# Kernel optimization log

Measured on AMD Instinct MI355X. Metric: run time of the kernel, lower is better.

Reference implementation:

```python
import math
import jax, jax.numpy as jnp
import numpy as np
from jax import lax

B, N, F = 16, 1024, 35  # graphs, nodes, one-hot label width
HID = 2000

def leaky(x):
    return jnp.where(x >= 0, x, 0.01 * x)

def spp(x, levels, mode):
    # x: [C,H,W]; faithful port of spatial_pyramid_pool.spp (per-level pool,
    # flatten, zero-pad to p*p). Pool params are static Python ints.
    C, H, W = x.shape
    outs = []
    for p in range(1, levels + 1):
        kh, kw = math.ceil(H / p), math.ceil(W / p)
        ph, pw = kh * p - H, kw * p - W
        if ph * 2 > kh:
            ph = kh // 2
        if pw * 2 > kw:
            pw = kw // 2
        pad = [(0, 0), (ph, ph), (pw, pw)]
        if mode == 'max':
            r = lax.reduce_window(x, -jnp.inf, lax.max, (1, kh, kw), (1, kh, kw), pad)
        else:  # avg, count_include_pad=True (torch default)
            r = lax.reduce_window(x, 0.0, lax.add, (1, kh, kw), (1, kh, kw), pad) / (kh * kw)
        flat = r.reshape(C, -1)
        flat = jnp.pad(flat, ((0, 0), (0, p * p - flat.shape[1])))
        outs.append(flat)
    return jnp.concatenate(outs, axis=1)  # [C, sum_p p^2]

def wlc(x, masks, K):
    # Vectorized weisfeiler_lehman_conv_switch.WLC.
    # x: [N,F]; masks: [4,N,N] one-hot of edge type s in {1..4}; K: [C,T,4,F].
    # Each convo step (snapshot semantics via cal_list.clone()):
    #   x_new[i] = x[i] + sum_j [s_ij==k+1] * x[j] * K[t,k]
    def one_channel(Kc):  # Kc: [T,4,F]
        def step(xc, Kt):
            return xc + jnp.einsum('kij,jf,kf->if', masks, xc, Kt), None
        xc, _ = lax.scan(step, x, Kc)
        return xc
    return jax.vmap(one_channel)(K)  # [C,N,F]

def conv2d(x, w, b):
    y = lax.conv_general_dilated(x, w, (1, 1), 'VALID',
                                 dimension_numbers=('NCHW', 'OIHW', 'NCHW'))
    return y + b[None, :, None, None]

def setup_inputs() -> dict:
    key = jax.random.key(0)
    ks = jax.random.split(key, 16)
    lin_in = 4 * sum((i + 1) ** 2 for i in range(10)) + 5 * sum((i + 1) ** 2 for i in range(3))  # 1610
    f32 = jnp.float32
    return {
        'labelsList': jax.random.normal(ks[0], (B, N, F), f32),
        'ligand_structure': jax.random.randint(ks[1], (B, N, N), 0, 5).astype(f32),
        'K1': jax.random.normal(ks[2], (2, 2, 4, F), f32) * 0.05,
        'K2': jax.random.normal(ks[3], (2, 2, 4, F), f32) * 0.05,
        'cw1': jax.random.normal(ks[4], (2, 1, 3, 3), f32) * 0.2,
        'cb1': jnp.zeros((2,), f32),
        'cw2': jax.random.normal(ks[5], (5, 2, 3, 3), f32) * 0.1,
        'cb2': jnp.zeros((5,), f32),
        'W1': jax.random.normal(ks[6], (HID, lin_in), f32) * 0.02,
        'b1': jnp.zeros((HID,), f32),
        'W2': jax.random.normal(ks[7], (HID, HID), f32) * 0.02,
        'b2': jnp.zeros((HID,), f32),
        'W3': jax.random.normal(ks[8], (HID, HID), f32) * 0.02,
        'b3': jnp.zeros((HID,), f32),
        'W4': jax.random.normal(ks[9], (HID, HID), f32) * 0.02,
        'b4': jnp.zeros((HID,), f32),
        'W5': jax.random.normal(ks[10], (2, HID), f32) * 0.02,
        'b5': jnp.zeros((2,), f32),
    }

def reference(labelsList, ligand_structure, K1, K2, cw1, cb1, cw2, cb2,
              W1, b1, W2, b2, W3, b3, W4, b4, W5, b5):
    def per_sample(x, s):  # x: [N,F], s: [N,N]
        masks = (s[None] == jnp.arange(1.0, 5.0, dtype=s.dtype)[:, None, None]).astype(x.dtype)
        c1 = leaky(wlc(x, masks, K1))                       # [2,N,F]
        c2 = jax.vmap(lambda xc: wlc(xc, masks, K2))(c1)    # [2,2,N,F], cat order matches torch
        c2 = c2.reshape(4, N, F)
        feat = spp(leaky(c2), 10, 'max').reshape(-1)        # [1540]
        z = s[None, None]                                   # [1,1,N,N]
        z = leaky(conv2d(z, cw1, cb1))
        z = leaky(conv2d(z, cw2, cb2))                      # [1,5,N-4,N-4]
        stru = spp(z[0], 3, 'avg').reshape(-1)              # [70]
        return jnp.concatenate([feat, stru])                # [1610]

    h = jax.vmap(per_sample)(labelsList, ligand_structure)  # [B,1610]
    # fc_model (dropout = identity in eval)
    h = leaky(h @ W1.T + b1)
    h = leaky(h @ W2.T + b2)
    h = leaky(h @ W3.T + b3)
    h = leaky(h @ W4.T + b4)
    return h @ W5.T + b5                                    # [B,2]
```

## Files before the change

kernel.cpp:

```cpp
#include <hip/hip_runtime.h>
#include <stdint.h>

#define NN 1024
#define FF 35
#define LIN_IN 1610
#define NB 16

typedef short short8 __attribute__((ext_vector_type(8)));
typedef float f32x4 __attribute__((ext_vector_type(4)));
typedef float f32x2 __attribute__((ext_vector_type(2)));

__device__ __forceinline__ float leakyf(float x) { return fmaxf(x, 0.01f * x); }
__device__ __forceinline__ uint16_t to_bf16(float v) {
    return (uint16_t)((__float_as_uint(v) + 0x8000u) >> 16);
}
__device__ __forceinline__ f32x2 sp2(float s) { return (f32x2){s, s}; }
__device__ __forceinline__ f32x2 leaky2(f32x2 v) {
    f32x2 r;
    r.x = fmaxf(v.x, 0.01f * v.x);
    r.y = fmaxf(v.y, 0.01f * v.y);
    return r;
}
__device__ __forceinline__ uint32_t mapf(float x) {
    uint32_t u = __float_as_uint(x);
    return (u & 0x80000000u) ? ~u : (u | 0x80000000u);
}
__device__ __forceinline__ float unmapf(uint32_t u) {
    return (u & 0x80000000u) ? __uint_as_float(u & 0x7FFFFFFFu) : __uint_as_float(~u);
}

__global__ __launch_bounds__(256)
void codes_kernel(const float* __restrict__ s, uint8_t* __restrict__ codes, int n4) {
    int i = blockIdx.x * 256 + threadIdx.x;
    for (; i < n4; i += gridDim.x * 256) {
        float4 v = ((const float4*)s)[i];
        uchar4 c;
        c.x = (uint8_t)v.x; c.y = (uint8_t)v.y; c.z = (uint8_t)v.z; c.w = (uint8_t)v.w;
        ((uchar4*)codes)[i] = c;
    }
}

__global__ __launch_bounds__(256)
void labels_to_xt(const float* __restrict__ labels, uint16_t* __restrict__ XT0,
                  float* __restrict__ XR0)
{
    __shared__ float buf[256 * FF];
    const int s = blockIdx.x;
    const int i0 = blockIdx.y * 256;
    const float* src = labels + ((size_t)s * NN + i0) * FF;
    for (int t = threadIdx.x; t < 256 * FF; t += 256) buf[t] = src[t];
    __syncthreads();
    for (int f = 0; f < 48; ++f) {
        const int ii = threadIdx.x;
        float v = (f < FF) ? buf[ii * FF + f] : 0.f;
        size_t o = ((size_t)s * 48 + f) * 1024 + i0 + ii;
        XR0[o] = v;
        XT0[o] = to_bf16(v);
    }
}

__device__ __forceinline__ short8 expand_onehot(uint2 cd, uint32_t dupK) {
    union { uint32_t u[4]; short8 v; } r;
#pragma unroll
    for (int h = 0; h < 2; ++h) {
        uint32_t d = h ? cd.y : cd.x;
        uint32_t y = d ^ dupK;
        uint32_t m = (~(((y & 0x7F7F7F7Fu) + 0x7F7F7F7Fu) | y)) & 0x80808080u;
        uint32_t m2 = m >> 7;
        r.u[h * 2 + 0] = ((m2 & 0xFFu) | ((m2 & 0xFF00u) << 8)) * 0x3F80u;
        r.u[h * 2 + 1] = (((m2 >> 16) & 0xFFu) | ((m2 >> 8) & 0xFF0000u)) * 0x3F80u;
    }
    return r.v;
}

__device__ __forceinline__
void wlc_body(int mt, int nt, int s,
              const uint16_t* __restrict__ XT_in, const float* __restrict__ XR_in,
              uint16_t* __restrict__ XT_out, float* __restrict__ XR_out,
              const uint8_t* __restrict__ codes, const float* __restrict__ Kg,
              int t, int shift, int nch_in, int nch_out, int do_leaky)
{
    const int tid   = threadIdx.x;
    const int wid   = tid >> 6;
    const int lane  = tid & 63;
    const int chout = nt;
    const int inch  = chout >> shift;
    const int kch   = chout & 1;
    const int i0    = mt * 64 + wid * 16;

    const uint8_t* cbase = codes + ((size_t)s << 20)
        + (size_t)(i0 + (lane & 15)) * 1024 + ((lane >> 4) << 3);
    const uint16_t* bbase = XT_in + (((size_t)s * nch_in + inch) * 48 + (lane & 15)) * 1024
        + ((lane >> 4) << 3);

    f32x4 acc[4][3];
#pragma unroll
    for (int k = 0; k < 4; ++k)
#pragma unroll
        for (int nf = 0; nf < 3; ++nf) acc[k][nf] = (f32x4){0.f, 0.f, 0.f, 0.f};

#pragma unroll 2
    for (int jt = 0; jt < 16; ++jt) {
        const int j0 = jt * 64;
        const uint2 cd0 = *(const uint2*)(cbase + j0);
        const uint2 cd1 = *(const uint2*)(cbase + j0 + 32);

        short8 bfr[3][2];
#pragma unroll
        for (int nf = 0; nf < 3; ++nf)
#pragma unroll
            for (int kk = 0; kk < 2; ++kk)
                bfr[nf][kk] = *(const short8*)(bbase + (size_t)nf * 16 * 1024 + j0 + kk * 32);

#pragma unroll
        for (int k = 0; k < 4; ++k) {
            const uint32_t dupK = 0x01010101u * (k + 1);
#pragma unroll
            for (int kk = 0; kk < 2; ++kk) {
                short8 af = expand_onehot(kk ? cd1 : cd0, dupK);
#pragma unroll
                for (int nf = 0; nf < 3; ++nf)
                    acc[k][nf] = __builtin_amdgcn_mfma_f32_16x16x32_bf16(
                        af, bfr[nf][kk], acc[k][nf], 0, 0, 0);
            }
        }
    }

    float sc[4][3];
#pragma unroll
    for (int nf = 0; nf < 3; ++nf) {
        int fnl = nf * 16 + (lane & 15);
#pragma unroll
        for (int k = 0; k < 4; ++k)
            sc[k][nf] = (fnl < FF) ? Kg[((kch * 2 + t) * 4 + k) * FF + fnl] : 0.f;
    }

#pragma unroll
    for (int nf = 0; nf < 3; ++nf) {
        int fnl = nf * 16 + (lane & 15);
        int irow = i0 + ((lane >> 4) << 2);
        f32x4 rr = sc[0][nf] * acc[0][nf];
        rr += sc[1][nf] * acc[1][nf];
        rr += sc[2][nf] * acc[2][nf];
        rr += sc[3][nf] * acc[3][nf];
        size_t rb = (((size_t)s * nch_in + inch) * 48 + fnl) * 1024 + irow;
        float4 rd = *(const float4*)&XR_in[rb];
        float y0 = rr.x + rd.x, y1 = rr.y + rd.y, y2 = rr.z + rd.z, y3 = rr.w + rd.w;
        if (do_leaky) { y0 = leakyf(y0); y1 = leakyf(y1); y2 = leakyf(y2); y3 = leakyf(y3); }
        size_t ob = (((size_t)s * nch_out + chout) * 48 + fnl) * 1024 + irow;
        *(float4*)&XR_out[ob] = make_float4(y0, y1, y2, y3);
        ushort4 bv;
        bv.x = to_bf16(y0); bv.y = to_bf16(y1); bv.z = to_bf16(y2); bv.w = to_bf16(y3);
        *(ushort4*)&XT_out[ob] = bv;
    }
}

__global__ __launch_bounds__(256, 2)
void wlc_gemm(const uint16_t* __restrict__ XT_in, const float* __restrict__ XR_in,
              uint16_t* __restrict__ XT_out, float* __restrict__ XR_out,
              const uint8_t* __restrict__ codes, const float* __restrict__ Kg,
              int t, int shift, int nch_in, int nch_out, int do_leaky)
{
    wlc_body(blockIdx.x, blockIdx.y, blockIdx.z, XT_in, XR_in, XT_out, XR_out,
             codes, Kg, t, shift, nch_in, nch_out, do_leaky);
}

__device__ __forceinline__
void conv_body(int ss, int simg,
               const float* __restrict__ sM,
               const float* __restrict__ cw1, const float* __restrict__ cb1,
               const float* __restrict__ cw2, const float* __restrict__ cb2,
               float* __restrict__ h0)
{
    __shared__ float bins[30];
    const int tid  = threadIdx.x;
    const int lane = tid & 63;
    const int r0   = ss * 17;
    const int rb2  = ss / 30;
    const int rb3  = ss / 20;

    if (tid < 30) bins[tid] = 0.f;
    __syncthreads();

    const int colbase = (tid < 255) ? tid * 4 : 254 * 4;
    const float* sp = sM + (size_t)simg * (NN * NN) + colbase;

    f32x2 w1p[9], w2p[45], b1p;
#pragma unroll
    for (int i = 0; i < 9; ++i) { w1p[i].x = cw1[i]; w1p[i].y = cw1[9 + i]; }
#pragma unroll
    for (int o = 0; o < 5; ++o)
#pragma unroll
        for (int i = 0; i < 9; ++i) {
            w2p[o * 9 + i].x = cw2[(o * 2 + 0) * 9 + i];
            w2p[o * 9 + i].y = cw2[(o * 2 + 1) * 9 + i];
        }
    b1p.x = cb1[0]; b1p.y = cb1[1];
    float b2r[5];
#pragma unroll
    for (int i = 0; i < 5; ++i) b2r[i] = cb2[i];

    float sw[3][8];
    f32x2 z1w[3][6];
    float acc[5][4];
#pragma unroll
    for (int o = 0; o < 5; ++o)
#pragma unroll
        for (int j = 0; j < 4; ++j) acc[o][j] = 0.f;

#define LOADROW(slot, rabs) do { \
    float4 v0 = *(const float4*)(sp + (size_t)(rabs) * NN); \
    float4 v1 = *(const float4*)(sp + (size_t)(rabs) * NN + 4); \
    sw[slot][0]=v0.x; sw[slot][1]=v0.y; sw[slot][2]=v0.z; sw[slot][3]=v0.w; \
    sw[slot][4]=v1.x; sw[slot][5]=v1.y; sw[slot][6]=v1.z; sw[slot][7]=v1.w; } while(0)

#define Z1ROW(P) do { \
    _Pragma("unroll") for (int jj = 0; jj < 6; ++jj) { \
        f32x2 a = b1p; \
        _Pragma("unroll") for (int dc = 0; dc < 3; ++dc) { \
            a += sp2(sw[((P)+2)%3][jj+dc]) * w1p[0+dc]; \
            a += sp2(sw[(P)%3    ][jj+dc]) * w1p[3+dc]; \
            a += sp2(sw[((P)+1)%3][jj+dc]) * w1p[6+dc]; } \
        z1w[((P)+2)%3][jj] = leaky2(a); } } while(0)

#define Z2ROW(P) do { \
    _Pragma("unroll") for (int o = 0; o < 5; ++o) { \
      _Pragma("unroll") for (int j = 0; j < 4; ++j) { \
        f32x2 a = (f32x2){b2r[o], 0.f}; \
        _Pragma("unroll") for (int dc = 0; dc < 3; ++dc) { \
            a += z1w[(P)%3    ][j+dc] * w2p[o*9+0+dc]; \
            a += z1w[((P)+1)%3][j+dc] * w2p[o*9+3+dc]; \
            a += z1w[((P)+2)%3][j+dc] * w2p[o*9+6+dc]; } \
        float sres = a.x + a.y; \
        acc[o][j] += fmaxf(sres, 0.01f * sres); } } } while(0)

    LOADROW(0, r0 + 0);
    LOADROW(1, r0 + 1);
    LOADROW(2, r0 + 2);
    Z1ROW(1);
    LOADROW(0, r0 + 3);
    Z1ROW(2);

#pragma unroll 1
    for (int rr = 0; rr < 15; rr += 3) {
        LOADROW(1, r0 + rr + 4); Z1ROW(0); Z2ROW(0);
        LOADROW(2, r0 + rr + 5); Z1ROW(1); Z2ROW(1);
        LOADROW(0, r0 + rr + 6); Z1ROW(2); Z2ROW(2);
    }
    LOADROW(1, r0 + 19); Z1ROW(0); Z2ROW(0);
    LOADROW(2, r0 + 20); Z1ROW(1); Z2ROW(1);

#undef LOADROW
#undef Z1ROW
#undef Z2ROW

    if (tid == 255) {
#pragma unroll
        for (int o = 0; o < 5; ++o)
#pragma unroll
            for (int j = 0; j < 4; ++j) acc[o][j] = 0.f;
    }

    int cb2c[4], cb3c[4];
#pragma unroll
    for (int j = 0; j < 4; ++j) {
        int col = colbase + j;
        int a2 = col / 510; if (a2 > 1) a2 = 1;
        int a3 = col / 340; if (a3 > 2) a3 = 2;
        cb2c[j] = a2; cb3c[j] = a3;
    }

#pragma unroll
    for (int o = 0; o < 5; ++o) {
        float t1 = acc[o][0] + acc[o][1] + acc[o][2] + acc[o][3];
        float pa = 0.f, pb = 0.f, q0 = 0.f, q1 = 0.f, q2 = 0.f;
#pragma unroll
        for (int j = 0; j < 4; ++j) {
            float v = acc[o][j];
            if (cb2c[j] == 0) pa += v; else pb += v;
            if (cb3c[j] == 0) q0 += v; else if (cb3c[j] == 1) q1 += v; else q2 += v;
        }
#pragma unroll
        for (int d = 32; d >= 1; d >>= 1) {
            t1 += __shfl_xor(t1, d, 64);
            pa += __shfl_xor(pa, d, 64);
            pb += __shfl_xor(pb, d, 64);
            q0 += __shfl_xor(q0, d, 64);
            q1 += __shfl_xor(q1, d, 64);
            q2 += __shfl_xor(q2, d, 64);
        }
        if (lane == 0) {
            atomicAdd(&bins[o * 6 + 0], t1);
            atomicAdd(&bins[o * 6 + 1], pa);
            atomicAdd(&bins[o * 6 + 2], pb);
            atomicAdd(&bins[o * 6 + 3], q0);
            atomicAdd(&bins[o * 6 + 4], q1);
            atomicAdd(&bins[o * 6 + 5], q2);
        }
    }
    __syncthreads();
    if (tid < 30) {
        int o = tid / 6, b = tid % 6;
        int off; float scale;
        if (b == 0)      { off = 0;                         scale = 1.f / (1020.f * 1020.f); }
        else if (b <= 2) { off = 1 + rb2 * 2 + (b - 1);     scale = 1.f / (510.f * 510.f); }
        else             { off = 5 + rb3 * 3 + (b - 3);     scale = 1.f / (340.f * 340.f); }
        atomicAdd(h0 + (size_t)simg * LIN_IN + 1540 + o * 14 + off, bins[tid] * scale);
    }
}

__global__ __launch_bounds__(256, 2)
void fused_wlc_conv(int convBlocks, int imgBase,
                    const float* __restrict__ sM,
                    const float* __restrict__ cw1, const float* __restrict__ cb1,
                    const float* __restrict__ cw2, const float* __restrict__ cb2,
                    float* __restrict__ h0,
                    const uint16_t* __restrict__ XT_in, const float* __restrict__ XR_in,
                    uint16_t* __restrict__ XT_out, float* __restrict__ XR_out,
                    const uint8_t* __restrict__ codes, const float* __restrict__ Kg,
                    int t, int shift, int nch_in, int nch_out, int do_leaky)
{
    const int bid = blockIdx.x;
    if (bid < convBlocks) {
        conv_body(bid % 60, imgBase + bid / 60, sM, cw1, cb1, cw2, cb2, h0);
    } else {
        const int b = bid - convBlocks;
        wlc_body(b & 15, (b >> 4) & 3, b >> 6, XT_in, XR_in, XT_out, XR_out,
                 codes, Kg, t, shift, nch_in, nch_out, do_leaky);
    }
}

__global__ __launch_bounds__(256)
void spp_scatter_kernel(const float* __restrict__ xr4, uint32_t* __restrict__ scratch)
{
    constexpr int KH[10] = {1024, 512, 342, 256, 205, 171, 147, 128, 114, 103};
    constexpr int PH[10] = {0, 0, 2, 0, 1, 2, 5, 0, 2, 6};
    constexpr int KW[10] = {35, 18, 12, 9, 7, 6, 5, 5, 4, 4};
    constexpr int PW[10] = {0, 1, 1, 1, 0, 1, 0, 2, 1, 2};
    constexpr int OW[10] = {1, 2, 3, 4, 5, 6, 7, 7, 9, 9};
    constexpr int BASE[10] = {0, 1, 5, 14, 30, 55, 91, 140, 204, 285};

    __shared__ uint32_t cells[385];
    const int b  = blockIdx.x;
    const int rq = b & 3;
    const int c  = (b >> 2) & 3;
    const int s  = b >> 4;
    const int r  = rq * 256 + threadIdx.x;

    for (int i = threadIdx.x; i < 385; i += 256) cells[i] = 0u;
    __syncthreads();

    const float* bp = xr4 + ((size_t)s * 4 + c) * (48 * 1024) + r;

    int addr[10];
#pragma unroll
    for (int pi = 0; pi < 10; ++pi)
        addr[pi] = BASE[pi] + ((r + PH[pi]) / KH[pi]) * OW[pi];

    float acc[10];
#pragma unroll
    for (int pi = 0; pi < 10; ++pi) acc[pi] = -3.402823466e38f;

#pragma unroll
    for (int f = 0; f < FF; ++f) {
        const float v = bp[(size_t)f * 1024];
#pragma unroll
        for (int pi = 0; pi < 10; ++pi) {
            const int cbin = (f + PW[pi]) / KW[pi];
            const int cbn  = (f + 1 < FF) ? ((f + 1 + PW[pi]) / KW[pi]) : -1;
            if (cbin < OW[pi]) {
                acc[pi] = fmaxf(acc[pi], v);
                if (cbn != cbin) {
                    atomicMax(&cells[addr[pi] + cbin], mapf(acc[pi]));
                    acc[pi] = -3.402823466e38f;
                }
            }
        }
    }

    __syncthreads();
    for (int i = threadIdx.x; i < 385; i += 256) {
        uint32_t u = cells[i];
        if (u) atomicMax(&scratch[((size_t)s * 4 + c) * 385 + i], u);
    }
}

__global__ __launch_bounds__(256)
void spp_unmap_kernel(const uint32_t* __restrict__ scratch, float* __restrict__ h0)
{
    constexpr int OHW[10] = {1, 4, 9, 16, 25, 36, 49, 56, 81, 90};
    const int idx = blockIdx.x * 256 + threadIdx.x;
    if (idx >= NB * 4 * 385) return;
    const int s = idx / (4 * 385);
    int rem = idx - s * (4 * 385);
    const int c = rem / 385;
    const int cell = rem - c * 385;

    int p1 = 1, base = 0;
    while (p1 < 10 && cell >= base + p1 * p1) { base += p1 * p1; ++p1; }
    const int ci = cell - base;
    if (ci >= OHW[p1 - 1]) return;

    h0[(size_t)s * LIN_IN + c * 385 + cell] = unmapf(scratch[idx]);
}

template<int VEC>
__global__ __launch_bounds__(256)
void fc_kernel(const float* __restrict__ in, const float* __restrict__ W,
               const float* __restrict__ bias, float* __restrict__ out,
               int K, int Nout, int do_leaky)
{
    const int o = (blockIdx.x * 256 + threadIdx.x) >> 6;
    const int lane = threadIdx.x & 63;
    if (o >= Nout) return;
    const float* wrow = W + (size_t)o * K;
    float acc[16];
#pragma unroll
    for (int b = 0; b < 16; ++b) acc[b] = 0.f;

    const int step = 64 * VEC;
    const int kmain = (K / step) * step;
#pragma unroll 2
    for (int k0 = 0; k0 < kmain; k0 += step) {
        const int kk = k0 + lane * VEC;
        if (VEC == 4) {
            float4 w = *(const float4*)(wrow + kk);
#pragma unroll
            for (int b = 0; b < 16; ++b) {
                float4 h = *(const float4*)(in + (size_t)b * K + kk);
                acc[b] += w.x * h.x + w.y * h.y + w.z * h.z + w.w * h.w;
            }
        } else {
            float2 w = *(const float2*)(wrow + kk);
#pragma unroll
            for (int b = 0; b < 16; ++b) {
                float2 h = *(const float2*)(in + (size_t)b * K + kk);
                acc[b] += w.x * h.x + w.y * h.y;
            }
        }
    }
    {
        const int kk = kmain + lane * VEC;
        if (kk < K) {
            if (VEC == 4) {
                float4 w = *(const float4*)(wrow + kk);
#pragma unroll
                for (int b = 0; b < 16; ++b) {
                    float4 h = *(const float4*)(in + (size_t)b * K + kk);
                    acc[b] += w.x * h.x + w.y * h.y + w.z * h.z + w.w * h.w;
                }
            } else {
                float2 w = *(const float2*)(wrow + kk);
#pragma unroll
                for (int b = 0; b < 16; ++b) {
                    float2 h = *(const float2*)(in + (size_t)b * K + kk);
                    acc[b] += w.x * h.x + w.y * h.y;
                }
            }
        }
    }

    float res = 0.f;
#pragma unroll
    for (int b = 0; b < 16; ++b) {
        float v = acc[b];
#pragma unroll
        for (int od = 32; od >= 1; od >>= 1) v += __shfl_xor(v, od, 64);
        if (lane == b) res = v;
    }
    if (lane < 16) {
        const float y = res + bias[o];
        out[(size_t)lane * Nout + o] = do_leaky ? leakyf(y) : y;
    }
}

extern "C" void kernel_launch(void* const* d_in, const int* in_sizes, int n_in,
                              void* d_out, int out_size, void* d_ws, size_t ws_size,
                              hipStream_t stream)
{
    const float* labels = (const float*)d_in[0];
    const float* sM     = (const float*)d_in[1];
    const float* K1     = (const float*)d_in[2];
    const float* K2     = (const float*)d_in[3];
    const float* cw1    = (const float*)d_in[4];
    const float* cb1    = (const float*)d_in[5];
    const float* cw2    = (const float*)d_in[6];
    const float* cb2    = (const float*)d_in[7];
    const float* W1     = (const float*)d_in[8];
    const float* b1     = (const float*)d_in[9];
    const float* W2     = (const float*)d_in[10];
    const float* b2     = (const float*)d_in[11];
    const float* W3     = (const float*)d_in[12];
    const float* b3     = (const float*)d_in[13];
    const float* W4     = (const float*)d_in[14];
    const float* b4     = (const float*)d_in[15];
    const float* W5     = (const float*)d_in[16];
    const float* b5     = (const float*)d_in[17];

    char* ws = (char*)d_ws;
    uint8_t* codes = (uint8_t*)ws;  ws += (size_t)16 << 20;
    char* ping = ws;                ws += 18874368;
    char* pong = ws;                ws += 18874368;
    float* h0  = (float*)ws;        ws += 103168;
    float* hA  = (float*)ws;        ws += 128000;
    float* hB  = (float*)ws;        ws += 128000;
    uint32_t* sppbuf = (uint32_t*)ws; ws += (size_t)NB * 4 * 385 * 4;

    uint16_t* XTp = (uint16_t*)ping; float* XRp = (float*)(ping + 6291456);
    uint16_t* XTq = (uint16_t*)pong; float* XRq = (float*)(pong + 6291456);

    hipMemsetAsync(h0, 0, (size_t)NB * LIN_IN * 4, stream);
    hipMemsetAsync(sppbuf, 0, (size_t)NB * 4 * 385 * 4, stream);

    codes_kernel<<<2048, 256, 0, stream>>>(sM, codes, 16 * 1024 * 1024 / 4);
    labels_to_xt<<<dim3(16, 4), 256, 0, stream>>>(labels, XTq, XRq);

    wlc_gemm<<<dim3(16, 2, 16), 256, 0, stream>>>(XTq, XRq, XTp, XRp, codes, K1, 0, 1, 1, 2, 0);
    wlc_gemm<<<dim3(16, 2, 16), 256, 0, stream>>>(XTp, XRp, XTq, XRq, codes, K1, 1, 0, 2, 2, 1);

    fused_wlc_conv<<<480 + 1024, 256, 0, stream>>>(
        480, 0, sM, cw1, cb1, cw2, cb2, h0,
        XTq, XRq, XTp, XRp, codes, K2, 0, 1, 2, 4, 0);
    fused_wlc_conv<<<480 + 1024, 256, 0, stream>>>(
        480, 8, sM, cw1, cb1, cw2, cb2, h0,
        XTp, XRp, XTq, XRq, codes, K2, 1, 0, 4, 4, 1);

    spp_scatter_kernel<<<256, 256, 0, stream>>>(XRq, sppbuf);
    spp_unmap_kernel<<<(NB * 4 * 385 + 255) / 256, 256, 0, stream>>>(sppbuf, h0);

    fc_kernel<2><<<500, 256, 0, stream>>>(h0, W1, b1, hA, LIN_IN, 2000, 1);
    fc_kernel<4><<<500, 256, 0, stream>>>(hA, W2, b2, hB, 2000, 2000, 1);
    fc_kernel<4><<<500, 256, 0, stream>>>(hB, W3, b3, hA, 2000, 2000, 1);
    fc_kernel<4><<<500, 256, 0, stream>>>(hA, W4, b4, hB, 2000, 2000, 1);
    fc_kernel<4><<<1,   256, 0, stream>>>(hB, W5, b5, (float*)d_out, 2000, 2, 0);
}
```

Before: 334.6 us.

## Stage WLC operands in LDS with prefetch, merge prep kernels, fuse SPP passes

The WLC GEMM body now stages each 64-wide slice of the bf16 feature tile and the edge-code tile in shared memory, using an XOR swizzle and register prefetch of the next slice. This replaces per-wave global loads, so the four waves share one copy. The codes and label-transpose kernels are merged into a single launch. The two-pass SPP (atomic scatter, then unmap) becomes one 1024-thread block per sample/channel that writes h0 directly, removing a memset and a launch. In exchange, the GEMM loop gains two barriers per iteration and uses more LDS, and the SPP kernel runs only 64 blocks.

```diff
diff --git a/kernel.cpp b/kernel.cpp
--- a/kernel.cpp
+++ b/kernel.cpp
@@ -30,32 +30,34 @@
 }
 
 __global__ __launch_bounds__(256)
-void codes_kernel(const float* __restrict__ s, uint8_t* __restrict__ codes, int n4) {
-    int i = blockIdx.x * 256 + threadIdx.x;
-    for (; i < n4; i += gridDim.x * 256) {
-        float4 v = ((const float4*)s)[i];
-        uchar4 c;
-        c.x = (uint8_t)v.x; c.y = (uint8_t)v.y; c.z = (uint8_t)v.z; c.w = (uint8_t)v.w;
-        ((uchar4*)codes)[i] = c;
-    }
-}
-
-__global__ __launch_bounds__(256)
-void labels_to_xt(const float* __restrict__ labels, uint16_t* __restrict__ XT0,
-                  float* __restrict__ XR0)
-{
-    __shared__ float buf[256 * FF];
-    const int s = blockIdx.x;
-    const int i0 = blockIdx.y * 256;
-    const float* src = labels + ((size_t)s * NN + i0) * FF;
-    for (int t = threadIdx.x; t < 256 * FF; t += 256) buf[t] = src[t];
-    __syncthreads();
-    for (int f = 0; f < 48; ++f) {
-        const int ii = threadIdx.x;
-        float v = (f < FF) ? buf[ii * FF + f] : 0.f;
-        size_t o = ((size_t)s * 48 + f) * 1024 + i0 + ii;
-        XR0[o] = v;
-        XT0[o] = to_bf16(v);
+void prep_kernel(const float* __restrict__ s, uint8_t* __restrict__ codes, int n4,
+                 const float* __restrict__ labels, uint16_t* __restrict__ XT0,
+                 float* __restrict__ XR0)
+{
+    const int bid = blockIdx.x;
+    if (bid < 2048) {
+        int i = bid * 256 + threadIdx.x;
+        for (; i < n4; i += 2048 * 256) {
+            float4 v = ((const float4*)s)[i];
+            uchar4 c;
+            c.x = (uint8_t)v.x; c.y = (uint8_t)v.y; c.z = (uint8_t)v.z; c.w = (uint8_t)v.w;
+            ((uchar4*)codes)[i] = c;
+        }
+    } else {
+        __shared__ float buf[256 * FF];
+        const int lb = bid - 2048;
+        const int si = lb >> 2;
+        const int i0 = (lb & 3) * 256;
+        const float* src = labels + ((size_t)si * NN + i0) * FF;
+        for (int t = threadIdx.x; t < 256 * FF; t += 256) buf[t] = src[t];
+        __syncthreads();
+        for (int f = 0; f < 48; ++f) {
+            const int ii = threadIdx.x;
+            float v = (f < FF) ? buf[ii * FF + f] : 0.f;
+            size_t o = ((size_t)si * 48 + f) * 1024 + i0 + ii;
+            XR0[o] = v;
+            XT0[o] = to_bf16(v);
+        }
     }
 }
 
@@ -80,18 +82,32 @@
               const uint8_t* __restrict__ codes, const float* __restrict__ Kg,
               int t, int shift, int nch_in, int nch_out, int do_leaky)
 {
+    __shared__ __align__(16) uint16_t xs[48 * 64];
+    __shared__ __align__(16) uint8_t  cds[64 * 80];
+
     const int tid   = threadIdx.x;
     const int wid   = tid >> 6;
     const int lane  = tid & 63;
     const int chout = nt;
     const int inch  = chout >> shift;
     const int kch   = chout & 1;
-    const int i0    = mt * 64 + wid * 16;
-
-    const uint8_t* cbase = codes + ((size_t)s << 20)
-        + (size_t)(i0 + (lane & 15)) * 1024 + ((lane >> 4) << 3);
-    const uint16_t* bbase = XT_in + (((size_t)s * nch_in + inch) * 48 + (lane & 15)) * 1024
-        + ((lane >> 4) << 3);
+    const int i0    = mt * 64;
+    const int irow0 = i0 + wid * 16;
+
+    const int u0 = tid, u1 = tid + 256;
+    const bool v1 = (u1 < 384);
+    const int r0s = u0 >> 3, c80 = u0 & 7;
+    const int r1s = u1 >> 3, c81 = u1 & 7;
+    const uint16_t* src0 = XT_in + (((size_t)s * nch_in + inch) * 48 + r0s) * 1024 + c80 * 8;
+    const uint16_t* src1 = XT_in + (((size_t)s * nch_in + inch) * 48 + (v1 ? r1s : 0)) * 1024 + c81 * 8;
+    uint16_t* dst0 = &xs[r0s * 64 + ((c80 ^ (r0s & 7)) * 8)];
+    uint16_t* dst1 = &xs[(v1 ? r1s : 0) * 64 + ((c81 ^ (r1s & 7)) * 8)];
+
+    const int crow = tid >> 2, ccol = (tid & 3) * 16;
+    const uint8_t* csrc = codes + ((size_t)s << 20) + (size_t)(i0 + crow) * 1024 + ccol;
+    uint8_t* cdst = &cds[crow * 80 + ccol];
+
+    const int cd_off = (wid * 16 + (lane & 15)) * 80 + ((lane >> 4) << 3);
 
     f32x4 acc[4][3];
 #pragma unroll
@@ -99,18 +115,36 @@
 #pragma unroll
         for (int nf = 0; nf < 3; ++nf) acc[k][nf] = (f32x4){0.f, 0.f, 0.f, 0.f};
 
-#pragma unroll 2
+    uint4 preB0 = *(const uint4*)src0;
+    uint4 preB1 = v1 ? *(const uint4*)src1 : (uint4){0, 0, 0, 0};
+    uint4 preC  = *(const uint4*)csrc;
+
     for (int jt = 0; jt < 16; ++jt) {
-        const int j0 = jt * 64;
-        const uint2 cd0 = *(const uint2*)(cbase + j0);
-        const uint2 cd1 = *(const uint2*)(cbase + j0 + 32);
+        __syncthreads();
+        *(uint4*)dst0 = preB0;
+        if (v1) *(uint4*)dst1 = preB1;
+        *(uint4*)cdst = preC;
+        __syncthreads();
+
+        if (jt < 15) {
+            const int j1 = (jt + 1) * 64;
+            preB0 = *(const uint4*)(src0 + j1);
+            if (v1) preB1 = *(const uint4*)(src1 + j1);
+            preC  = *(const uint4*)(csrc + j1);
+        }
+
+        const uint2 cd0 = *(const uint2*)&cds[cd_off];
+        const uint2 cd1 = *(const uint2*)&cds[cd_off + 32];
 
         short8 bfr[3][2];
 #pragma unroll
         for (int nf = 0; nf < 3; ++nf)
 #pragma unroll
-            for (int kk = 0; kk < 2; ++kk)
-                bfr[nf][kk] = *(const short8*)(bbase + (size_t)nf * 16 * 1024 + j0 + kk * 32);
+            for (int kk = 0; kk < 2; ++kk) {
+                int n = nf * 16 + (lane & 15);
+                int c8 = kk * 4 + (lane >> 4);
+                bfr[nf][kk] = *(const short8*)&xs[n * 64 + ((c8 ^ (n & 7)) * 8)];
+            }
 
 #pragma unroll
         for (int k = 0; k < 4; ++k) {
@@ -138,7 +172,7 @@
 #pragma unroll
     for (int nf = 0; nf < 3; ++nf) {
         int fnl = nf * 16 + (lane & 15);
-        int irow = i0 + ((lane >> 4) << 2);
+        int irow = irow0 + ((lane >> 4) << 2);
         f32x4 rr = sc[0][nf] * acc[0][nf];
         rr += sc[1][nf] * acc[1][nf];
         rr += sc[2][nf] * acc[2][nf];
@@ -324,30 +358,29 @@
     if (bid < convBlocks) {
         conv_body(bid % 60, imgBase + bid / 60, sM, cw1, cb1, cw2, cb2, h0);
     } else {
-        const int b = bid - convBlocks;
-        wlc_body(b & 15, (b >> 4) & 3, b >> 6, XT_in, XR_in, XT_out, XR_out,
+        const int w = bid - convBlocks;
+        wlc_body(w & 15, (w >> 4) & 3, w >> 6, XT_in, XR_in, XT_out, XR_out,
                  codes, Kg, t, shift, nch_in, nch_out, do_leaky);
     }
 }
 
-__global__ __launch_bounds__(256)
-void spp_scatter_kernel(const float* __restrict__ xr4, uint32_t* __restrict__ scratch)
+__global__ __launch_bounds__(1024)
+void spp_kernel(const float* __restrict__ xr4, float* __restrict__ h0)
 {
     constexpr int KH[10] = {1024, 512, 342, 256, 205, 171, 147, 128, 114, 103};
     constexpr int PH[10] = {0, 0, 2, 0, 1, 2, 5, 0, 2, 6};
     constexpr int KW[10] = {35, 18, 12, 9, 7, 6, 5, 5, 4, 4};
     constexpr int PW[10] = {0, 1, 1, 1, 0, 1, 0, 2, 1, 2};
     constexpr int OW[10] = {1, 2, 3, 4, 5, 6, 7, 7, 9, 9};
+    constexpr int OHW[10] = {1, 4, 9, 16, 25, 36, 49, 56, 81, 90};
     constexpr int BASE[10] = {0, 1, 5, 14, 30, 55, 91, 140, 204, 285};
 
     __shared__ uint32_t cells[385];
-    const int b  = blockIdx.x;
-    const int rq = b & 3;
-    const int c  = (b >> 2) & 3;
-    const int s  = b >> 4;
-    const int r  = rq * 256 + threadIdx.x;
-
-    for (int i = threadIdx.x; i < 385; i += 256) cells[i] = 0u;
+    const int c = blockIdx.x & 3;
+    const int s = blockIdx.x >> 2;
+    const int r = threadIdx.x;
+
+    if (r < 385) cells[r] = 0u;
     __syncthreads();
 
     const float* bp = xr4 + ((size_t)s * 4 + c) * (48 * 1024) + r;
@@ -379,29 +412,13 @@
     }
 
     __syncthreads();
-    for (int i = threadIdx.x; i < 385; i += 256) {
-        uint32_t u = cells[i];
-        if (u) atomicMax(&scratch[((size_t)s * 4 + c) * 385 + i], u);
-    }
-}
-
-__global__ __launch_bounds__(256)
-void spp_unmap_kernel(const uint32_t* __restrict__ scratch, float* __restrict__ h0)
-{
-    constexpr int OHW[10] = {1, 4, 9, 16, 25, 36, 49, 56, 81, 90};
-    const int idx = blockIdx.x * 256 + threadIdx.x;
-    if (idx >= NB * 4 * 385) return;
-    const int s = idx / (4 * 385);
-    int rem = idx - s * (4 * 385);
-    const int c = rem / 385;
-    const int cell = rem - c * 385;
-
-    int p1 = 1, base = 0;
-    while (p1 < 10 && cell >= base + p1 * p1) { base += p1 * p1; ++p1; }
-    const int ci = cell - base;
-    if (ci >= OHW[p1 - 1]) return;
-
-    h0[(size_t)s * LIN_IN + c * 385 + cell] = unmapf(scratch[idx]);
+    if (r < 385) {
+        int p1 = 1, base = 0;
+        while (p1 < 10 && r >= base + p1 * p1) { base += p1 * p1; ++p1; }
+        const int ci = r - base;
+        const float val = (ci < OHW[p1 - 1]) ? unmapf(cells[r]) : 0.f;
+        h0[(size_t)s * LIN_IN + c * 385 + r] = val;
+    }
 }
 
 template<int VEC>
@@ -504,16 +521,14 @@
     float* h0  = (float*)ws;        ws += 103168;
     float* hA  = (float*)ws;        ws += 128000;
     float* hB  = (float*)ws;        ws += 128000;
-    uint32_t* sppbuf = (uint32_t*)ws; ws += (size_t)NB * 4 * 385 * 4;
 
     uint16_t* XTp = (uint16_t*)ping; float* XRp = (float*)(ping + 6291456);
     uint16_t* XTq = (uint16_t*)pong; float* XRq = (float*)(pong + 6291456);
 
     hipMemsetAsync(h0, 0, (size_t)NB * LIN_IN * 4, stream);
-    hipMemsetAsync(sppbuf, 0, (size_t)NB * 4 * 385 * 4, stream);
-
-    codes_kernel<<<2048, 256, 0, stream>>>(sM, codes, 16 * 1024 * 1024 / 4);
-    labels_to_xt<<<dim3(16, 4), 256, 0, stream>>>(labels, XTq, XRq);
+
+    prep_kernel<<<2048 + 64, 256, 0, stream>>>(sM, codes, 16 * 1024 * 1024 / 4,
+                                               labels, XTq, XRq);
 
     wlc_gemm<<<dim3(16, 2, 16), 256, 0, stream>>>(XTq, XRq, XTp, XRp, codes, K1, 0, 1, 1, 2, 0);
     wlc_gemm<<<dim3(16, 2, 16), 256, 0, stream>>>(XTp, XRp, XTq, XRq, codes, K1, 1, 0, 2, 2, 1);
@@ -525,8 +540,7 @@
         480, 8, sM, cw1, cb1, cw2, cb2, h0,
         XTp, XRp, XTq, XRq, codes, K2, 1, 0, 4, 4, 1);
 
-    spp_scatter_kernel<<<256, 256, 0, stream>>>(XRq, sppbuf);
-    spp_unmap_kernel<<<(NB * 4 * 385 + 255) / 256, 256, 0, stream>>>(sppbuf, h0);
+    spp_kernel<<<64, 1024, 0, stream>>>(XRq, h0);
 
     fc_kernel<2><<<500, 256, 0, stream>>>(h0, W1, b1, hA, LIN_IN, 2000, 1);
     fc_kernel<4><<<500, 256, 0, stream>>>(hA, W2, b2, hB, 2000, 2000, 1);
```

Result: faster. 313.5 us (-6.3%).
